# Kernel optimization log

Measured on AMD Instinct MI355X. Metric: run time of the kernel, lower is better.

Reference implementation:

```python
import jax, jax.numpy as jnp
import numpy as np
from jax.scipy.special import logsumexp

# cfg.LOSS constants
BLUR = 0.01
REACH = 0.5
P = 1
SCALE = 0.6          # global `scale` used by exp_cost
CROP = 512
DS = 8               # downsample_ratio
TAU = 0.1
N_ITERS = 30         # fixed-iteration log-domain Sinkhorn (geomloss scaling=0.9 surrogate)
EPS = BLUR ** P      # blur**p
RHO = REACH ** P     # unbalanced mass penalty


def make_grid(H, W):
    # grid(H, W, 1) * DS + DS/2, then / CROP  (exactly mirrors the torch code)
    coodx = jnp.arange(0, W, dtype=jnp.float32) + 0.5
    coody = jnp.arange(0, H, dtype=jnp.float32) + 0.5
    ys, xs = jnp.meshgrid(coody, coodx, indexing='ij')
    g = jnp.stack((xs, ys), axis=2).reshape(-1, 2)            # [H*W, 2], (x, y)
    return (g * DS + DS / 2) / float(CROP)


def exp_cost(X, Y):
    # X: [B,N,2], Y: [B,M,2]  ->  C: [B,N,M]
    D2 = jnp.sum((X[:, :, None, :] - Y[:, None, :, :]) ** 2, axis=-1)
    C = jnp.sqrt(D2 + 1e-12)
    return jnp.exp(C / SCALE) - 1.0


def sinkhorn_potentials(log_a, C):
    # Unbalanced log-domain Sinkhorn with uniform unit target weights (gt = 1).
    # log_a: [B,N] (detached), C: [B,N,M] (detached). Returns f:[B,N], g:[B,M].
    B, N = log_a.shape
    M = C.shape[2]
    damping = RHO / (RHO + EPS)

    def body(_, fg):
        f, g = fg
        g = -EPS * damping * logsumexp(log_a[:, :, None] + (f[:, :, None] - C) / EPS, axis=1)
        f = -EPS * damping * logsumexp((g[:, None, :] - C) / EPS, axis=2)  # log_b = 0
        return (f, g)

    f0 = jnp.zeros((B, N), C.dtype)
    g0 = jnp.zeros((B, M), C.dtype)
    return jax.lax.fori_loop(0, N_ITERS, body, (f0, g0))


def setup_inputs() -> dict:
    key = jax.random.key(0)
    k1, k2 = jax.random.split(key)
    H = W = CROP // DS  # 64
    predict_map = jax.random.uniform(k1, (8, 1, H, W), dtype=jnp.float32)
    points = jax.random.uniform(k2, (8, 512, 2), dtype=jnp.float32) * float(CROP)
    return {"predict_map": predict_map, "points": points}


def reference(predict_map, points):
    B, _, H, W = predict_map.shape
    N = H * W
    cood_grid = make_grid(H, W)                               # [N,2]
    X = jnp.broadcast_to(cood_grid[None], (B, N, 2))
    Y = points / float(CROP)                                  # [B,M,2]
    A = predict_map.reshape(B, N)                             # pixel masses

    C = exp_cost(X, Y)                                        # [B,N,M]
    Cd = jax.lax.stop_gradient(C)
    log_a = jax.lax.stop_gradient(jnp.log(A + 1e-20))

    f, g = sinkhorn_potentials(log_a, Cd)
    f = jax.lax.stop_gradient(f)
    g = jax.lax.stop_gradient(g)

    # unbalanced OT loss per sample (debias=False): rho*<a, 1-e^{-f/rho}> + rho*<b, 1-e^{-g/rho}>
    l = RHO * jnp.sum(A * (1.0 - jnp.exp(-f / RHO)), axis=1) \
      + RHO * jnp.sum(1.0 - jnp.exp(-g / RHO), axis=1)        # [B]

    # transport plan: exp((F + G - C).detach() / blur**p) * A * gt^T  (gt = 1)
    PI = jnp.exp((f[:, :, None] + g[:, None, :] - Cd) / EPS) * A[:, :, None]  # [B,N,M]

    entropy = jnp.sum(jnp.mean((1e-20 + PI) * jnp.log(1e-20 + PI), axis=(1, 2)))
    emd_loss = jnp.sum(l)
    point_loss = jnp.sum(jnp.abs(jnp.sum(PI, axis=1) - 1.0))                      # d_point = l1
    pixel_loss = jnp.sum(jnp.abs(jax.lax.stop_gradient(jnp.sum(PI, axis=2)) - A)) # d_pixel = l1

    counting_loss = emd_loss + TAU * (pixel_loss + point_loss) + BLUR * entropy
    return counting_loss
```

## Files before the change

### kernel.cpp

```cpp
#include <hip/hip_runtime.h>
#include <math.h>

#define ITERS 30

#define WS_F    0
#define WS_G    32768
#define WS_LA   36864
#define WS_P1   69632
#define WS_P2   72704

__device__ __forceinline__ float fexp2(float x){ return __builtin_amdgcn_exp2f(x); }
__device__ __forceinline__ float flog2(float x){ return __builtin_amdgcn_logf(x); }
__device__ __forceinline__ float fsq(float x){ return __builtin_amdgcn_sqrtf(x); }

__device__ __forceinline__ float wave_max(float v){
  #pragma unroll
  for (int off = 1; off < 64; off <<= 1) v = fmaxf(v, __shfl_xor(v, off));
  return v;
}
__device__ __forceinline__ float wave_sum(float v){
  #pragma unroll
  for (int off = 1; off < 64; off <<= 1) v += __shfl_xor(v, off);
  return v;
}

__device__ const float LN2f   = 0.69314718055994530942f;
__device__ const float INVLN2 = 1.44269504088896340736f;
__device__ const float K2     = 2.40449173481494868463f;
__device__ const float KC     = 144.269504088896340736f;
__device__ const float CNEG   = -0.0067955605937249540f;
__device__ const float IRHOL2 = 2.88539008177792681472f;

__global__ __launch_bounds__(256) void k_init(const float* __restrict__ A, float* __restrict__ ws){
  int i = blockIdx.x * 256 + threadIdx.x;
  if (i < 32768){
    ws[WS_F + i] = 0.f;
    ws[WS_LA + i] = LN2f * flog2(A[i] + 1e-20f);
  }
  if (i < 4096) ws[WS_G + i] = 0.f;
}

__global__ __launch_bounds__(256) void k_gupd(const float* __restrict__ pts, float* __restrict__ ws){
  __shared__ float P[4096];
  int blk = blockIdx.x;
  int b = blk >> 7;
  int mt = blk & 127;
  const float4* f4  = (const float4*)(ws + WS_F  + b*4096);
  const float4* la4 = (const float4*)(ws + WS_LA + b*4096);
  for (int k = threadIdx.x; k < 1024; k += 256){
    float4 fv = f4[k], lv = la4[k];
    float4 o;
    o.x = (lv.x + 100.f*fv.x + 100.f) * INVLN2;
    o.y = (lv.y + 100.f*fv.y + 100.f) * INVLN2;
    o.z = (lv.z + 100.f*fv.z + 100.f) * INVLN2;
    o.w = (lv.w + 100.f*fv.w + 100.f) * INVLN2;
    ((float4*)P)[k] = o;
  }
  __syncthreads();
  int w = threadIdx.x >> 6, l = threadIdx.x & 63;
  int m = mt*4 + w;
  float ymx = pts[(b*512 + m)*2 + 0] * (1.f/512.f);
  float ymy = pts[(b*512 + m)*2 + 1] * (1.f/512.f);
  float xn  = (float)(l + 1) * (1.f/64.f);
  float dx  = xn - ymx;
  float dx2 = __builtin_fmaf(dx, dx, 1e-12f);
  float mrun = -INFINITY, srun = 0.f;
  #pragma unroll
  for (int c = 0; c < 4; ++c){
    float x[16];
    float cm = -INFINITY;
    #pragma unroll
    for (int jj = 0; jj < 16; ++jj){
      int j = c*16 + jj;
      float yn = (float)(j + 1) * (1.f/64.f);
      float dy = yn - ymy;
      float d2 = __builtin_fmaf(dy, dy, dx2);
      float E  = fexp2(fsq(d2) * K2);
      float y  = __builtin_fmaf(-KC, E, P[j*64 + l]);
      x[jj] = y;
      cm = fmaxf(cm, y);
    }
    float mnew = fmaxf(mrun, cm);
    float cs = 0.f;
    #pragma unroll
    for (int jj = 0; jj < 16; ++jj) cs += fexp2(x[jj] - mnew);
    srun = __builtin_fmaf(srun, fexp2(mrun - mnew), cs);
    mrun = mnew;
  }
  float Mx = wave_max(mrun);
  float S  = wave_sum(srun * fexp2(mrun - Mx));
  if (l == 0)
    ws[WS_G + b*512 + m] = CNEG * (Mx + flog2(S));
}

__global__ __launch_bounds__(256) void k_fupd(const float* __restrict__ pts, float* __restrict__ ws){
  __shared__ float4 Q[512];
  int blk = blockIdx.x;
  int b = blk >> 7;
  int nt = blk & 127;
  const float*  g  = ws + WS_G + b*512;
  const float2* p2 = (const float2*)(pts + b*1024);
  for (int m = threadIdx.x; m < 512; m += 256){
    float2 pv = p2[m];
    Q[m] = make_float4(__builtin_fmaf(g[m], KC, KC), pv.x*(1.f/512.f), pv.y*(1.f/512.f), 0.f);
  }
  __syncthreads();
  int w = threadIdx.x >> 6, l = threadIdx.x & 63;
  #pragma unroll 1
  for (int r = 0; r < 8; ++r){
    int n = nt*32 + w*8 + r;
    float xn = (float)((n & 63) + 1) * (1.f/64.f);
    float yn = (float)((n >> 6) + 1) * (1.f/64.f);
    float x[8]; float cm = -INFINITY;
    #pragma unroll
    for (int jm = 0; jm < 8; ++jm){
      float4 q = Q[jm*64 + l];
      float dxx = q.y - xn, dyy = q.z - yn;
      float d2 = __builtin_fmaf(dyy, dyy, __builtin_fmaf(dxx, dxx, 1e-12f));
      float E  = fexp2(fsq(d2) * K2);
      float y  = __builtin_fmaf(-KC, E, q.x);
      x[jm] = y; cm = fmaxf(cm, y);
    }
    float Mx = wave_max(cm);
    float s = 0.f;
    #pragma unroll
    for (int jm = 0; jm < 8; ++jm) s += fexp2(x[jm] - Mx);
    float S = wave_sum(s);
    if (l == 0)
      ws[WS_F + b*4096 + n] = CNEG * (Mx + flog2(S));
  }
}

__global__ __launch_bounds__(256) void k_ep1(const float* __restrict__ A, const float* __restrict__ pts, float* __restrict__ ws){
  __shared__ float4 Q[512];
  __shared__ float red[12];
  int blk = blockIdx.x;
  int b = blk >> 7;
  int nt = blk & 127;
  const float*  g  = ws + WS_G + b*512;
  const float*  f  = ws + WS_F + b*4096;
  const float*  Ab = A + b*4096;
  const float2* p2 = (const float2*)(pts + b*1024);
  for (int m = threadIdx.x; m < 512; m += 256){
    float2 pv = p2[m];
    Q[m] = make_float4(__builtin_fmaf(g[m], KC, KC), pv.x*(1.f/512.f), pv.y*(1.f/512.f), 0.f);
  }
  __syncthreads();
  int w = threadIdx.x >> 6, l = threadIdx.x & 63;
  float ent = 0.f, pix = 0.f, emdf = 0.f;
  #pragma unroll 1
  for (int r = 0; r < 8; ++r){
    int n = nt*32 + w*8 + r;
    float fn = f[n], An = Ab[n];
    float F2 = fn * KC;
    float xn = (float)((n & 63) + 1) * (1.f/64.f);
    float yn = (float)((n >> 6) + 1) * (1.f/64.f);
    float rs = 0.f;
    #pragma unroll
    for (int jm = 0; jm < 8; ++jm){
      float4 q = Q[jm*64 + l];
      float dxx = q.y - xn, dyy = q.z - yn;
      float d2 = __builtin_fmaf(dyy, dyy, __builtin_fmaf(dxx, dxx, 1e-12f));
      float E  = fexp2(fsq(d2) * K2);
      float z  = F2 + __builtin_fmaf(-KC, E, q.x);
      float p  = fexp2(z) * An;
      rs += p;
      float qq = p + 1e-20f;
      ent = __builtin_fmaf(qq, LN2f * flog2(qq), ent);
    }
    rs = wave_sum(rs);
    if (l == 0){
      pix  += fabsf(rs - An);
      emdf += An * (1.f - fexp2(fn * -IRHOL2));
    }
  }
  ent = wave_sum(ent); pix = wave_sum(pix); emdf = wave_sum(emdf);
  if (l == 0){ red[w*3+0] = ent; red[w*3+1] = pix; red[w*3+2] = emdf; }
  __syncthreads();
  if (threadIdx.x == 0){
    float e = 0.f, p = 0.f, q = 0.f;
    for (int i = 0; i < 4; ++i){ e += red[i*3]; p += red[i*3+1]; q += red[i*3+2]; }
    float* P1 = ws + WS_P1;
    P1[blk*3+0] = e; P1[blk*3+1] = p; P1[blk*3+2] = q;
  }
}

__global__ __launch_bounds__(256) void k_ep2(const float* __restrict__ A, const float* __restrict__ pts, float* __restrict__ ws){
  __shared__ float Wn[4096];
  __shared__ float red[8];
  int blk = blockIdx.x;
  int b = blk >> 7;
  int mt = blk & 127;
  const float4* f4 = (const float4*)(ws + WS_F + b*4096);
  const float4* A4 = (const float4*)(A + b*4096);
  for (int k = threadIdx.x; k < 1024; k += 256){
    float4 fv = f4[k], av = A4[k];
    float4 o;
    o.x = __builtin_fmaf(fv.x, KC, flog2(av.x));
    o.y = __builtin_fmaf(fv.y, KC, flog2(av.y));
    o.z = __builtin_fmaf(fv.z, KC, flog2(av.z));
    o.w = __builtin_fmaf(fv.w, KC, flog2(av.w));
    ((float4*)Wn)[k] = o;
  }
  __syncthreads();
  int w = threadIdx.x >> 6, l = threadIdx.x & 63;
  int m = mt*4 + w;
  float gm  = ws[WS_G + b*512 + m];
  float G2  = __builtin_fmaf(gm, KC, KC);
  float ymx = pts[(b*512 + m)*2 + 0] * (1.f/512.f);
  float ymy = pts[(b*512 + m)*2 + 1] * (1.f/512.f);
  float xn  = (float)(l + 1) * (1.f/64.f);
  float dx  = xn - ymx;
  float dx2 = __builtin_fmaf(dx, dx, 1e-12f);
  float cs = 0.f;
  #pragma unroll
  for (int j = 0; j < 64; ++j){
    float yn = (float)(j + 1) * (1.f/64.f);
    float dy = yn - ymy;
    float d2 = __builtin_fmaf(dy, dy, dx2);
    float E  = fexp2(fsq(d2) * K2);
    float z  = G2 + __builtin_fmaf(-KC, E, Wn[j*64 + l]);
    cs += fexp2(z);
  }
  cs = wave_sum(cs);
  if (l == 0){
    red[w*2+0] = fabsf(cs - 1.f);
    red[w*2+1] = 1.f - fexp2(gm * -IRHOL2);
  }
  __syncthreads();
  if (threadIdx.x == 0){
    float p = 0.f, e = 0.f;
    for (int i = 0; i < 4; ++i){ p += red[i*2]; e += red[i*2+1]; }
    float* P2 = ws + WS_P2;
    P2[blk*2+0] = p; P2[blk*2+1] = e;
  }
}

__global__ __launch_bounds__(256) void k_fin(const float* __restrict__ ws, float* __restrict__ out){
  __shared__ float red[20];
  float e = 0.f, pix = 0.f, emdf = 0.f, pnt = 0.f, emdg = 0.f;
  for (int i = threadIdx.x; i < 1024; i += 256){
    e    += ws[WS_P1 + i*3 + 0];
    pix  += ws[WS_P1 + i*3 + 1];
    emdf += ws[WS_P1 + i*3 + 2];
    pnt  += ws[WS_P2 + i*2 + 0];
    emdg += ws[WS_P2 + i*2 + 1];
  }
  e = wave_sum(e); pix = wave_sum(pix); emdf = wave_sum(emdf);
  pnt = wave_sum(pnt); emdg = wave_sum(emdg);
  int w = threadIdx.x >> 6, l = threadIdx.x & 63;
  if (l == 0){
    red[w*5+0] = e; red[w*5+1] = pix; red[w*5+2] = emdf; red[w*5+3] = pnt; red[w*5+4] = emdg;
  }
  __syncthreads();
  if (threadIdx.x == 0){
    float E = 0.f, PX = 0.f, EF = 0.f, PT = 0.f, EG = 0.f;
    for (int i = 0; i < 4; ++i){
      E += red[i*5]; PX += red[i*5+1]; EF += red[i*5+2]; PT += red[i*5+3]; EG += red[i*5+4];
    }
    float emd = 0.5f * (EF + EG);
    float entropy = E * (1.f / (4096.f * 512.f));
    out[0] = emd + 0.1f * (PX + PT) + 0.01f * entropy;
  }
}

extern "C" void kernel_launch(void* const* d_in, const int* in_sizes, int n_in,
                              void* d_out, int out_size, void* d_ws, size_t ws_size,
                              hipStream_t stream) {
  const float* A   = (const float*)d_in[0];
  const float* pts = (const float*)d_in[1];
  float* ws  = (float*)d_ws;
  float* out = (float*)d_out;

  k_init<<<128, 256, 0, stream>>>(A, ws);
  for (int it = 0; it < ITERS; ++it){
    k_gupd<<<1024, 256, 0, stream>>>(pts, ws);
    k_fupd<<<1024, 256, 0, stream>>>(pts, ws);
  }
  k_ep1<<<1024, 256, 0, stream>>>(A, pts, ws);
  k_ep2<<<1024, 256, 0, stream>>>(A, pts, ws);
  k_fin<<<1, 256, 0, stream>>>(ws, out);
}
```

Before: 641.9 us.

## Fuse Sinkhorn iterations into one persistent kernel with per-batch grid barriers

Replaces the 60+ per-iteration kernel launches with one persistent kernel of 256 blocks (32 per batch). Each thread keeps its slice of the cost matrix in registers, computed once instead of every iteration. Blocks in a batch synchronise through atomic-counter barriers in workspace, and the epilogue losses are folded into the same kernel. This removes launch overhead and repeated cost recomputation, but relies on all blocks being co-resident. It adds heavy register pressure (64-element array per thread) and a spin-wait with a timeout break that could silently give wrong results.

```diff
diff --git a/kernel.cpp b/kernel.cpp
--- a/kernel.cpp
+++ b/kernel.cpp
@@ -3,11 +3,17 @@
 
 #define ITERS 30
 
-#define WS_F    0
-#define WS_G    32768
-#define WS_LA   36864
-#define WS_P1   69632
-#define WS_P2   72704
+#define PEND  1024
+#define GBUF  132096
+#define BPART 136192
+
+#define LN2f    0.69314718055994530942f
+#define INVLN2  1.44269504088896340736f
+#define K2c     2.40449173481494868463f
+#define KCc     144.269504088896340736f
+#define RKCc    0.0069314718055994530942f
+#define CNEGc  -0.0067955605937249540f
+#define IRHOL2c 2.88539008177792681472f
 
 __device__ __forceinline__ float fexp2(float x){ return __builtin_amdgcn_exp2f(x); }
 __device__ __forceinline__ float flog2(float x){ return __builtin_amdgcn_logf(x); }
@@ -24,243 +30,193 @@
   return v;
 }
 
-__device__ const float LN2f   = 0.69314718055994530942f;
-__device__ const float INVLN2 = 1.44269504088896340736f;
-__device__ const float K2     = 2.40449173481494868463f;
-__device__ const float KC     = 144.269504088896340736f;
-__device__ const float CNEG   = -0.0067955605937249540f;
-__device__ const float IRHOL2 = 2.88539008177792681472f;
-
-__global__ __launch_bounds__(256) void k_init(const float* __restrict__ A, float* __restrict__ ws){
-  int i = blockIdx.x * 256 + threadIdx.x;
-  if (i < 32768){
-    ws[WS_F + i] = 0.f;
-    ws[WS_LA + i] = LN2f * flog2(A[i] + 1e-20f);
-  }
-  if (i < 4096) ws[WS_G + i] = 0.f;
-}
-
-__global__ __launch_bounds__(256) void k_gupd(const float* __restrict__ pts, float* __restrict__ ws){
-  __shared__ float P[4096];
-  int blk = blockIdx.x;
-  int b = blk >> 7;
-  int mt = blk & 127;
-  const float4* f4  = (const float4*)(ws + WS_F  + b*4096);
-  const float4* la4 = (const float4*)(ws + WS_LA + b*4096);
-  for (int k = threadIdx.x; k < 1024; k += 256){
-    float4 fv = f4[k], lv = la4[k];
-    float4 o;
-    o.x = (lv.x + 100.f*fv.x + 100.f) * INVLN2;
-    o.y = (lv.y + 100.f*fv.y + 100.f) * INVLN2;
-    o.z = (lv.z + 100.f*fv.z + 100.f) * INVLN2;
-    o.w = (lv.w + 100.f*fv.w + 100.f) * INVLN2;
-    ((float4*)P)[k] = o;
-  }
-  __syncthreads();
-  int w = threadIdx.x >> 6, l = threadIdx.x & 63;
-  int m = mt*4 + w;
-  float ymx = pts[(b*512 + m)*2 + 0] * (1.f/512.f);
-  float ymy = pts[(b*512 + m)*2 + 1] * (1.f/512.f);
-  float xn  = (float)(l + 1) * (1.f/64.f);
-  float dx  = xn - ymx;
-  float dx2 = __builtin_fmaf(dx, dx, 1e-12f);
-  float mrun = -INFINITY, srun = 0.f;
-  #pragma unroll
-  for (int c = 0; c < 4; ++c){
-    float x[16];
-    float cm = -INFINITY;
-    #pragma unroll
-    for (int jj = 0; jj < 16; ++jj){
-      int j = c*16 + jj;
-      float yn = (float)(j + 1) * (1.f/64.f);
-      float dy = yn - ymy;
-      float d2 = __builtin_fmaf(dy, dy, dx2);
-      float E  = fexp2(fsq(d2) * K2);
-      float y  = __builtin_fmaf(-KC, E, P[j*64 + l]);
-      x[jj] = y;
-      cm = fmaxf(cm, y);
-    }
-    float mnew = fmaxf(mrun, cm);
-    float cs = 0.f;
-    #pragma unroll
-    for (int jj = 0; jj < 16; ++jj) cs += fexp2(x[jj] - mnew);
-    srun = __builtin_fmaf(srun, fexp2(mrun - mnew), cs);
-    mrun = mnew;
-  }
-  float Mx = wave_max(mrun);
-  float S  = wave_sum(srun * fexp2(mrun - Mx));
-  if (l == 0)
-    ws[WS_G + b*512 + m] = CNEG * (Mx + flog2(S));
-}
-
-__global__ __launch_bounds__(256) void k_fupd(const float* __restrict__ pts, float* __restrict__ ws){
-  __shared__ float4 Q[512];
-  int blk = blockIdx.x;
-  int b = blk >> 7;
-  int nt = blk & 127;
-  const float*  g  = ws + WS_G + b*512;
-  const float2* p2 = (const float2*)(pts + b*1024);
-  for (int m = threadIdx.x; m < 512; m += 256){
-    float2 pv = p2[m];
-    Q[m] = make_float4(__builtin_fmaf(g[m], KC, KC), pv.x*(1.f/512.f), pv.y*(1.f/512.f), 0.f);
-  }
-  __syncthreads();
-  int w = threadIdx.x >> 6, l = threadIdx.x & 63;
+__device__ __forceinline__ void bar_sync(int* c, int target){
+  __syncthreads();
+  if (threadIdx.x == 0){
+    __hip_atomic_fetch_add(c, 1, __ATOMIC_ACQ_REL, __HIP_MEMORY_SCOPE_AGENT);
+    int spins = 0;
+    while (__hip_atomic_load(c, __ATOMIC_ACQUIRE, __HIP_MEMORY_SCOPE_AGENT) < target){
+      __builtin_amdgcn_s_sleep(1);
+      if (++spins > (1 << 22)) break;
+    }
+  }
+  __syncthreads();
+}
+
+__global__ __launch_bounds__(1024, 4) void k_sink(const float* __restrict__ A,
+                                                  const float* __restrict__ pts,
+                                                  float* __restrict__ ws,
+                                                  float* __restrict__ out){
+  __shared__ float2 pms[512 * 17];
+  __shared__ float red[80];
+  const int tid = threadIdx.x, w = tid >> 6, l = tid & 63;
+  const int bb = blockIdx.x, b = bb >> 5, s = bb & 31;
+  int* cnt  = (int*)ws;
+  int* cbat = cnt + b * 64;
+
+  float nK[64];
+  float laK[8], P[8], G2[8], y[8];
+
+  {
+    float px[8], py[8];
+    #pragma unroll
+    for (int k = 0; k < 8; ++k){
+      int m = k * 64 + l;
+      px[k] = pts[(b*512 + m)*2 + 0] * (1.f/512.f);
+      py[k] = pts[(b*512 + m)*2 + 1] * (1.f/512.f);
+    }
+    #pragma unroll
+    for (int r = 0; r < 8; ++r){
+      int n = s*128 + w*8 + r;
+      float xn = (float)((n & 63) + 1) * (1.f/64.f);
+      float yn = (float)((n >> 6) + 1) * (1.f/64.f);
+      laK[r] = flog2(A[b*4096 + n] + 1e-20f) + KCc;
+      P[r]   = laK[r];
+      #pragma unroll
+      for (int k = 0; k < 8; ++k){
+        float dx = xn - px[k], dy = yn - py[k];
+        float d2 = __builtin_fmaf(dy, dy, __builtin_fmaf(dx, dx, 1e-12f));
+        nK[r*8 + k] = -KCc * fexp2(fsq(d2) * K2c);
+      }
+    }
+  }
+
   #pragma unroll 1
+  for (int it = 0; it < ITERS; ++it){
+    #pragma unroll
+    for (int k = 0; k < 8; ++k){
+      float pm = -INFINITY;
+      #pragma unroll
+      for (int r = 0; r < 8; ++r){ y[r] = P[r] + nK[r*8 + k]; pm = fmaxf(pm, y[r]); }
+      float ps = 0.f;
+      #pragma unroll
+      for (int r = 0; r < 8; ++r) ps += fexp2(y[r] - pm);
+      pms[(k*64 + l)*17 + w] = make_float2(pm, ps);
+    }
+    __syncthreads();
+    if (tid < 512){
+      int m = tid;
+      float M = -INFINITY;
+      #pragma unroll
+      for (int q = 0; q < 16; ++q) M = fmaxf(M, pms[m*17 + q].x);
+      float S = 0.f;
+      #pragma unroll
+      for (int q = 0; q < 16; ++q){ float2 v = pms[m*17 + q]; S += v.y * fexp2(v.x - M); }
+      ws[PEND + (b*32 + s)*512 + m] = M + flog2(S);
+    }
+    bar_sync(cbat + 2*it, 32);
+
+    {
+      int mc = s*16 + w;
+      float L = (l < 32) ? ws[PEND + (b*32 + l)*512 + mc] : -INFINITY;
+      float M = wave_max(L);
+      float S = wave_sum((l < 32) ? fexp2(L - M) : 0.f);
+      float g = CNEGc * (M + flog2(S));
+      if (l == 0) ws[GBUF + b*512 + mc] = g;
+    }
+    bar_sync(cbat + 2*it + 1, 32);
+
+    #pragma unroll
+    for (int k = 0; k < 8; ++k)
+      G2[k] = __builtin_fmaf(ws[GBUF + b*512 + k*64 + l], KCc, KCc);
+    #pragma unroll
+    for (int r = 0; r < 8; ++r){
+      float cm = -INFINITY;
+      #pragma unroll
+      for (int k = 0; k < 8; ++k){ y[k] = G2[k] + nK[r*8 + k]; cm = fmaxf(cm, y[k]); }
+      float M = wave_max(cm);
+      float sv = 0.f;
+      #pragma unroll
+      for (int k = 0; k < 8; ++k) sv += fexp2(y[k] - M);
+      float S = wave_sum(sv);
+      float f = CNEGc * (M + flog2(S));
+      P[r] = __builtin_fmaf(f, KCc, laK[r]);
+    }
+  }
+
+  float ent = 0.f, pix = 0.f, emdf = 0.f, csum[8];
+  #pragma unroll
+  for (int k = 0; k < 8; ++k) csum[k] = 0.f;
+  #pragma unroll
   for (int r = 0; r < 8; ++r){
-    int n = nt*32 + w*8 + r;
-    float xn = (float)((n & 63) + 1) * (1.f/64.f);
-    float yn = (float)((n >> 6) + 1) * (1.f/64.f);
-    float x[8]; float cm = -INFINITY;
-    #pragma unroll
-    for (int jm = 0; jm < 8; ++jm){
-      float4 q = Q[jm*64 + l];
-      float dxx = q.y - xn, dyy = q.z - yn;
-      float d2 = __builtin_fmaf(dyy, dyy, __builtin_fmaf(dxx, dxx, 1e-12f));
-      float E  = fexp2(fsq(d2) * K2);
-      float y  = __builtin_fmaf(-KC, E, q.x);
-      x[jm] = y; cm = fmaxf(cm, y);
-    }
-    float Mx = wave_max(cm);
-    float s = 0.f;
-    #pragma unroll
-    for (int jm = 0; jm < 8; ++jm) s += fexp2(x[jm] - Mx);
-    float S = wave_sum(s);
-    if (l == 0)
-      ws[WS_F + b*4096 + n] = CNEG * (Mx + flog2(S));
-  }
-}
-
-__global__ __launch_bounds__(256) void k_ep1(const float* __restrict__ A, const float* __restrict__ pts, float* __restrict__ ws){
-  __shared__ float4 Q[512];
-  __shared__ float red[12];
-  int blk = blockIdx.x;
-  int b = blk >> 7;
-  int nt = blk & 127;
-  const float*  g  = ws + WS_G + b*512;
-  const float*  f  = ws + WS_F + b*4096;
-  const float*  Ab = A + b*4096;
-  const float2* p2 = (const float2*)(pts + b*1024);
-  for (int m = threadIdx.x; m < 512; m += 256){
-    float2 pv = p2[m];
-    Q[m] = make_float4(__builtin_fmaf(g[m], KC, KC), pv.x*(1.f/512.f), pv.y*(1.f/512.f), 0.f);
-  }
-  __syncthreads();
-  int w = threadIdx.x >> 6, l = threadIdx.x & 63;
-  float ent = 0.f, pix = 0.f, emdf = 0.f;
-  #pragma unroll 1
-  for (int r = 0; r < 8; ++r){
-    int n = nt*32 + w*8 + r;
-    float fn = f[n], An = Ab[n];
-    float F2 = fn * KC;
-    float xn = (float)((n & 63) + 1) * (1.f/64.f);
-    float yn = (float)((n >> 6) + 1) * (1.f/64.f);
+    float base = P[r] - KCc;
+    float An   = fexp2(laK[r] - KCc);
+    float fr   = (P[r] - laK[r]) * RKCc;
     float rs = 0.f;
     #pragma unroll
-    for (int jm = 0; jm < 8; ++jm){
-      float4 q = Q[jm*64 + l];
-      float dxx = q.y - xn, dyy = q.z - yn;
-      float d2 = __builtin_fmaf(dyy, dyy, __builtin_fmaf(dxx, dxx, 1e-12f));
-      float E  = fexp2(fsq(d2) * K2);
-      float z  = F2 + __builtin_fmaf(-KC, E, q.x);
-      float p  = fexp2(z) * An;
-      rs += p;
-      float qq = p + 1e-20f;
-      ent = __builtin_fmaf(qq, LN2f * flog2(qq), ent);
-    }
-    rs = wave_sum(rs);
+    for (int k = 0; k < 8; ++k){
+      float z = base + G2[k] + nK[r*8 + k];
+      float p = fexp2(z);
+      rs += p; csum[k] += p;
+      float q = p + 1e-20f;
+      ent = __builtin_fmaf(q * LN2f, flog2(q), ent);
+    }
+    float RS = wave_sum(rs);
     if (l == 0){
-      pix  += fabsf(rs - An);
-      emdf += An * (1.f - fexp2(fn * -IRHOL2));
-    }
+      pix  += fabsf(RS - An);
+      emdf += An * (1.f - fexp2(fr * -IRHOL2c));
+    }
+  }
+  float* pmsf = (float*)pms;
+  #pragma unroll
+  for (int k = 0; k < 8; ++k) pmsf[(k*64 + l)*17 + w] = csum[k];
+  __syncthreads();
+  if (tid < 512){
+    float cb = 0.f;
+    #pragma unroll
+    for (int q = 0; q < 16; ++q) cb += pmsf[tid*17 + q];
+    ws[PEND + (b*32 + s)*512 + tid] = cb;
+  }
+  bar_sync(cbat + 60, 32);
+
+  float pnt = 0.f;
+  {
+    int mc = s*16 + w;
+    float v = (l < 32) ? ws[PEND + (b*32 + l)*512 + mc] : 0.f;
+    float CS = wave_sum(v);
+    if (l == 0) pnt = fabsf(CS - 1.f);
+  }
+  float emdg = 0.f;
+  if (s == 0 && tid < 512){
+    float g = ws[GBUF + b*512 + tid];
+    emdg = 1.f - fexp2(g * -IRHOL2c);
   }
   ent = wave_sum(ent); pix = wave_sum(pix); emdf = wave_sum(emdf);
-  if (l == 0){ red[w*3+0] = ent; red[w*3+1] = pix; red[w*3+2] = emdf; }
-  __syncthreads();
-  if (threadIdx.x == 0){
-    float e = 0.f, p = 0.f, q = 0.f;
-    for (int i = 0; i < 4; ++i){ e += red[i*3]; p += red[i*3+1]; q += red[i*3+2]; }
-    float* P1 = ws + WS_P1;
-    P1[blk*3+0] = e; P1[blk*3+1] = p; P1[blk*3+2] = q;
-  }
-}
-
-__global__ __launch_bounds__(256) void k_ep2(const float* __restrict__ A, const float* __restrict__ pts, float* __restrict__ ws){
-  __shared__ float Wn[4096];
-  __shared__ float red[8];
-  int blk = blockIdx.x;
-  int b = blk >> 7;
-  int mt = blk & 127;
-  const float4* f4 = (const float4*)(ws + WS_F + b*4096);
-  const float4* A4 = (const float4*)(A + b*4096);
-  for (int k = threadIdx.x; k < 1024; k += 256){
-    float4 fv = f4[k], av = A4[k];
-    float4 o;
-    o.x = __builtin_fmaf(fv.x, KC, flog2(av.x));
-    o.y = __builtin_fmaf(fv.y, KC, flog2(av.y));
-    o.z = __builtin_fmaf(fv.z, KC, flog2(av.z));
-    o.w = __builtin_fmaf(fv.w, KC, flog2(av.w));
-    ((float4*)Wn)[k] = o;
-  }
-  __syncthreads();
-  int w = threadIdx.x >> 6, l = threadIdx.x & 63;
-  int m = mt*4 + w;
-  float gm  = ws[WS_G + b*512 + m];
-  float G2  = __builtin_fmaf(gm, KC, KC);
-  float ymx = pts[(b*512 + m)*2 + 0] * (1.f/512.f);
-  float ymy = pts[(b*512 + m)*2 + 1] * (1.f/512.f);
-  float xn  = (float)(l + 1) * (1.f/64.f);
-  float dx  = xn - ymx;
-  float dx2 = __builtin_fmaf(dx, dx, 1e-12f);
-  float cs = 0.f;
-  #pragma unroll
-  for (int j = 0; j < 64; ++j){
-    float yn = (float)(j + 1) * (1.f/64.f);
-    float dy = yn - ymy;
-    float d2 = __builtin_fmaf(dy, dy, dx2);
-    float E  = fexp2(fsq(d2) * K2);
-    float z  = G2 + __builtin_fmaf(-KC, E, Wn[j*64 + l]);
-    cs += fexp2(z);
-  }
-  cs = wave_sum(cs);
+  pnt = wave_sum(pnt); emdg = wave_sum(emdg);
   if (l == 0){
-    red[w*2+0] = fabsf(cs - 1.f);
-    red[w*2+1] = 1.f - fexp2(gm * -IRHOL2);
-  }
-  __syncthreads();
-  if (threadIdx.x == 0){
-    float p = 0.f, e = 0.f;
-    for (int i = 0; i < 4; ++i){ p += red[i*2]; e += red[i*2+1]; }
-    float* P2 = ws + WS_P2;
-    P2[blk*2+0] = p; P2[blk*2+1] = e;
-  }
-}
-
-__global__ __launch_bounds__(256) void k_fin(const float* __restrict__ ws, float* __restrict__ out){
-  __shared__ float red[20];
-  float e = 0.f, pix = 0.f, emdf = 0.f, pnt = 0.f, emdg = 0.f;
-  for (int i = threadIdx.x; i < 1024; i += 256){
-    e    += ws[WS_P1 + i*3 + 0];
-    pix  += ws[WS_P1 + i*3 + 1];
-    emdf += ws[WS_P1 + i*3 + 2];
-    pnt  += ws[WS_P2 + i*2 + 0];
-    emdg += ws[WS_P2 + i*2 + 1];
-  }
-  e = wave_sum(e); pix = wave_sum(pix); emdf = wave_sum(emdf);
-  pnt = wave_sum(pnt); emdg = wave_sum(emdg);
-  int w = threadIdx.x >> 6, l = threadIdx.x & 63;
-  if (l == 0){
-    red[w*5+0] = e; red[w*5+1] = pix; red[w*5+2] = emdf; red[w*5+3] = pnt; red[w*5+4] = emdg;
-  }
-  __syncthreads();
-  if (threadIdx.x == 0){
-    float E = 0.f, PX = 0.f, EF = 0.f, PT = 0.f, EG = 0.f;
-    for (int i = 0; i < 4; ++i){
-      E += red[i*5]; PX += red[i*5+1]; EF += red[i*5+2]; PT += red[i*5+3]; EG += red[i*5+4];
-    }
-    float emd = 0.5f * (EF + EG);
-    float entropy = E * (1.f / (4096.f * 512.f));
-    out[0] = emd + 0.1f * (PX + PT) + 0.01f * entropy;
+    red[w*5+0] = ent; red[w*5+1] = pix; red[w*5+2] = emdf; red[w*5+3] = pnt; red[w*5+4] = emdg;
+  }
+  __syncthreads();
+  if (tid == 0){
+    float a0=0,a1=0,a2=0,a3=0,a4=0;
+    for (int q = 0; q < 16; ++q){
+      a0 += red[q*5+0]; a1 += red[q*5+1]; a2 += red[q*5+2]; a3 += red[q*5+3]; a4 += red[q*5+4];
+    }
+    float* bp = ws + BPART + bb*8;
+    bp[0]=a0; bp[1]=a1; bp[2]=a2; bp[3]=a3; bp[4]=a4;
+  }
+
+  bar_sync(cnt + 512, 256);
+
+  if (bb == 0){
+    float v0=0,v1=0,v2=0,v3=0,v4=0;
+    if (tid < 256){
+      const float* bp = ws + BPART + tid*8;
+      v0=bp[0]; v1=bp[1]; v2=bp[2]; v3=bp[3]; v4=bp[4];
+    }
+    v0=wave_sum(v0); v1=wave_sum(v1); v2=wave_sum(v2); v3=wave_sum(v3); v4=wave_sum(v4);
+    if (l == 0){
+      red[w*5+0]=v0; red[w*5+1]=v1; red[w*5+2]=v2; red[w*5+3]=v3; red[w*5+4]=v4;
+    }
+    __syncthreads();
+    if (tid == 0){
+      float E=0,PX=0,EF=0,PT=0,EG=0;
+      for (int q = 0; q < 16; ++q){
+        E += red[q*5+0]; PX += red[q*5+1]; EF += red[q*5+2]; PT += red[q*5+3]; EG += red[q*5+4];
+      }
+      float emd = 0.5f * (EF + EG);
+      out[0] = emd + 0.1f * (PX + PT) + 0.01f * (E * (1.f / (4096.f * 512.f)));
+    }
   }
 }
 
@@ -272,12 +228,6 @@
   float* ws  = (float*)d_ws;
   float* out = (float*)d_out;
 
-  k_init<<<128, 256, 0, stream>>>(A, ws);
-  for (int it = 0; it < ITERS; ++it){
-    k_gupd<<<1024, 256, 0, stream>>>(pts, ws);
-    k_fupd<<<1024, 256, 0, stream>>>(pts, ws);
-  }
-  k_ep1<<<1024, 256, 0, stream>>>(A, pts, ws);
-  k_ep2<<<1024, 256, 0, stream>>>(A, pts, ws);
-  k_fin<<<1, 256, 0, stream>>>(ws, out);
-}
+  hipMemsetAsync(d_ws, 0, 4096, stream);
+  k_sink<<<256, 1024, 0, stream>>>(A, pts, ws, out);
+}
```

Measured after the change: 868.9 us. 1.35x slower.
